# Performance work log

Measured on AMD Instinct MI355X. Metric: run time of the kernel, lower is better.

## Reference

```python
import jax, jax.numpy as jnp
import numpy as np

TAU = 1.0            # temperature (self.temperature.item())
FAST_WEIGHT_DECAY = 0.01
FAST_WEIGHT_LR = 0.01

B, IN, H = 128, 1024, 1024


def setup_inputs() -> dict:
    key = jax.random.key(0)
    k = jax.random.split(key, 6)
    scale_ih = 1.0 / np.sqrt(IN)
    scale_hh = np.sqrt(2.0 / (H + H))  # xavier_uniform-like std
    return {
        "x_t": jax.random.normal(k[0], (B, IN), jnp.float32),
        "h_prev": jax.random.normal(k[1], (B, H), jnp.float32),
        "W_ih": jax.random.normal(k[2], (H, IN), jnp.float32) * scale_ih,
        "b_ih": jnp.zeros((H,), jnp.float32),
        "W_hh_fixed": jax.random.normal(k[3], (H, H), jnp.float32) * scale_hh,
        "W_hh_virtual": jnp.zeros((H, H), jnp.float32),
        "gumbel_u": jax.random.uniform(k[4], (B, H, H), jnp.float32),
    }


def reference(x_t, h_prev, W_ih, b_ih, W_hh_fixed, W_hh_virtual, gumbel_u):
    # input contribution: Linear(input_size, hidden_size)
    input_contrib = x_t @ W_ih.T + b_ih                      # (B, H)

    # logits scaled by temperature once, then gumbel_softmax divides by tau again
    logits = (W_hh_fixed + W_hh_virtual) / TAU               # (H, H)
    eps = 1e-9
    g = -jnp.log(-jnp.log(jnp.clip(gumbel_u, eps, 1.0 - eps)))  # Gumbel(0,1), (B,H,H)
    y = jax.nn.softmax((logits[None, :, :] + g) / TAU, axis=2)  # soft sampling, (B,H,H)

    # weighted exchange: each output neuron o reduces sampled weights against h_prev
    contrib = jnp.einsum('boh,bh->bo', y, h_prev)            # (B, H)
    h_next = jnp.tanh(input_contrib + contrib)               # (B, H)

    # Hebbian fast-weight update (no_grad in original)
    hebbian = jnp.einsum('bo,bh->oh', h_next, h_prev) / B    # mean over batch, (H,H)
    W_hh_virtual_new = jax.lax.stop_gradient(
        W_hh_virtual * (1.0 - FAST_WEIGHT_DECAY) + hebbian * FAST_WEIGHT_LR
    )
    return h_next, W_hh_virtual_new
```

## Files before the change

kernel.cpp:

```cpp
#include <hip/hip_runtime.h>
#include <hip/hip_bf16.h>
#include <cstddef>

#define B_DIM  128
#define IN_DIM 1024
#define H_DIM  1024

constexpr float kDecay   = 1.0f - 0.01f;
constexpr float kLrOverB = 0.01f / 128.0f;

__global__ __launch_bounds__(256) void exp_logits(
    const float* __restrict__ W_f,
    const float* __restrict__ W_v,
    float* __restrict__ E)
{
    const int i = blockIdx.x * 256 + threadIdx.x;
    const float4 a = reinterpret_cast<const float4*>(W_f)[i];
    const float4 b = reinterpret_cast<const float4*>(W_v)[i];
    float4 e;
    e.x = __expf(a.x + b.x); e.y = __expf(a.y + b.y);
    e.z = __expf(a.z + b.z); e.w = __expf(a.w + b.w);
    reinterpret_cast<float4*>(E)[i] = e;
}

__global__ __launch_bounds__(256) void input_gemm(
    const float* __restrict__ x_t,
    const float* __restrict__ W_ih,
    const float* __restrict__ b_ih,
    float* __restrict__ ic)
{
    const int o0 = blockIdx.x * 64;
    const int b0 = blockIdx.y * 16;
    const int t  = threadIdx.x;

    __shared__ float Wt[64][68];
    __shared__ float xs[64][17];

    const int tx = t & 15;
    const int ty = t >> 4;

    float acc[4] = {0.f, 0.f, 0.f, 0.f};

    for (int kc = 0; kc < IN_DIM / 64; ++kc) {
        const int k0 = kc * 64;

#pragma unroll
        for (int ii = 0; ii < 4; ++ii) {
            const int i  = t + 256 * ii;
            const int r  = i >> 4;
            const int c4 = (i & 15) * 4;
            const float4 wv = *reinterpret_cast<const float4*>(
                &W_ih[(size_t)(o0 + r) * IN_DIM + k0 + c4]);
            Wt[c4 + 0][r] = wv.x; Wt[c4 + 1][r] = wv.y;
            Wt[c4 + 2][r] = wv.z; Wt[c4 + 3][r] = wv.w;
        }
        {
            const int br = t >> 4;
            const int c4 = (t & 15) * 4;
            const float4 xv = *reinterpret_cast<const float4*>(
                &x_t[(size_t)(b0 + br) * IN_DIM + k0 + c4]);
            xs[c4 + 0][br] = xv.x; xs[c4 + 1][br] = xv.y;
            xs[c4 + 2][br] = xv.z; xs[c4 + 3][br] = xv.w;
        }
        __syncthreads();

#pragma unroll 8
        for (int k = 0; k < 64; ++k) {
            const float  xb = xs[k][ty];
            const float4 wv = *reinterpret_cast<const float4*>(&Wt[k][4 * tx]);
            acc[0] = fmaf(wv.x, xb, acc[0]);
            acc[1] = fmaf(wv.y, xb, acc[1]);
            acc[2] = fmaf(wv.z, xb, acc[2]);
            acc[3] = fmaf(wv.w, xb, acc[3]);
        }
        __syncthreads();
    }

    const int o = o0 + 4 * tx;
    const int b = b0 + ty;
    float4 r;
    r.x = acc[0] + b_ih[o + 0];
    r.y = acc[1] + b_ih[o + 1];
    r.z = acc[2] + b_ih[o + 2];
    r.w = acc[3] + b_ih[o + 3];
    *reinterpret_cast<float4*>(&ic[(size_t)b * H_DIM + o]) = r;
}

__global__ __launch_bounds__(256) void fused_rows(
    const float* __restrict__ h_prev,
    const float* __restrict__ E,
    const float* __restrict__ gu,
    const float* __restrict__ ic,
    float* __restrict__ h_next)
{
    const int b    = blockIdx.y;
    const int t    = threadIdx.x;
    const int w    = t >> 6;
    const int lane = t & 63;
    const int ob   = blockIdx.x * 32 + w * 8;

    const float4* hp4 = reinterpret_cast<const float4*>(h_prev + (size_t)b * H_DIM);
    float4 hp[4];
#pragma unroll
    for (int j = 0; j < 4; ++j) hp[j] = hp4[lane + 64 * j];

    const float4* g4 = reinterpret_cast<const float4*>(gu + ((size_t)b * H_DIM + ob) * H_DIM);
    const float4* e4 = reinterpret_cast<const float4*>(E + (size_t)ob * H_DIM);

    float s[8], d[8];

#pragma unroll
    for (int r = 0; r < 8; ++r) {
        float sum = 0.f, dot = 0.f;
#pragma unroll
        for (int j = 0; j < 4; ++j) {
            const int idx = r * 256 + lane + 64 * j;
            const float4 u = g4[idx];
            const float4 e = e4[idx];
            const float4 p = hp[j];

            const float q0 = __fdividef(e.x, -__log2f(fmaxf(u.x, 1e-9f)));
            const float q1 = __fdividef(e.y, -__log2f(fmaxf(u.y, 1e-9f)));
            const float q2 = __fdividef(e.z, -__log2f(fmaxf(u.z, 1e-9f)));
            const float q3 = __fdividef(e.w, -__log2f(fmaxf(u.w, 1e-9f)));

            sum += (q0 + q1) + (q2 + q3);
            dot = fmaf(q0, p.x, dot);
            dot = fmaf(q1, p.y, dot);
            dot = fmaf(q2, p.z, dot);
            dot = fmaf(q3, p.w, dot);
        }
        s[r] = sum;
        d[r] = dot;
    }

#pragma unroll
    for (int off = 32; off > 0; off >>= 1) {
#pragma unroll
        for (int r = 0; r < 8; ++r) {
            s[r] += __shfl_xor(s[r], off, 64);
            d[r] += __shfl_xor(d[r], off, 64);
        }
    }

    if (lane == 0) {
        const size_t base = (size_t)b * H_DIM + ob;
        const float4 i0 = *reinterpret_cast<const float4*>(ic + base);
        const float4 i1 = *reinterpret_cast<const float4*>(ic + base + 4);
        float4 r0, r1;
        r0.x = tanhf(i0.x + __fdividef(d[0], s[0]));
        r0.y = tanhf(i0.y + __fdividef(d[1], s[1]));
        r0.z = tanhf(i0.z + __fdividef(d[2], s[2]));
        r0.w = tanhf(i0.w + __fdividef(d[3], s[3]));
        r1.x = tanhf(i1.x + __fdividef(d[4], s[4]));
        r1.y = tanhf(i1.y + __fdividef(d[5], s[5]));
        r1.z = tanhf(i1.z + __fdividef(d[6], s[6]));
        r1.w = tanhf(i1.w + __fdividef(d[7], s[7]));
        *reinterpret_cast<float4*>(h_next + base)     = r0;
        *reinterpret_cast<float4*>(h_next + base + 4) = r1;
    }
}

__global__ __launch_bounds__(256) void hebbian_update(
    const float* __restrict__ h_next,
    const float* __restrict__ h_prev,
    const float* __restrict__ W_v,
    float* __restrict__ W_out)
{
    const int h0 = blockIdx.x * 64;
    const int o0 = blockIdx.y * 64;
    const int t  = threadIdx.x;

    __shared__ __align__(16) float hn_s[B_DIM][64];
    __shared__ __align__(16) float hp_s[B_DIM][64];

#pragma unroll
    for (int i = 0; i < 32; ++i) {
        const int e  = t + 256 * i;
        const int bb = e >> 6;
        const int cc = e & 63;
        hn_s[bb][cc] = h_next[(size_t)bb * H_DIM + o0 + cc];
        hp_s[bb][cc] = h_prev[(size_t)bb * H_DIM + h0 + cc];
    }
    __syncthreads();

    const int tx = t & 15;
    const int ty = t >> 4;

    float acc[4][4] = {{0.f}};

#pragma unroll 8
    for (int b = 0; b < B_DIM; ++b) {
        const float4 av = reinterpret_cast<const float4*>(hn_s[b])[ty];
        const float4 bv = reinterpret_cast<const float4*>(hp_s[b])[tx];
        const float aa[4] = {av.x, av.y, av.z, av.w};
        const float bb[4] = {bv.x, bv.y, bv.z, bv.w};
#pragma unroll
        for (int a = 0; a < 4; ++a)
#pragma unroll
            for (int c = 0; c < 4; ++c)
                acc[a][c] = fmaf(aa[a], bb[c], acc[a][c]);
    }

#pragma unroll
    for (int a = 0; a < 4; ++a) {
        const int o = o0 + 4 * ty + a;
        const size_t base = (size_t)o * H_DIM + h0 + 4 * tx;
        const float4 wv = *reinterpret_cast<const float4*>(W_v + base);
        float4 r;
        r.x = wv.x * kDecay + acc[a][0] * kLrOverB;
        r.y = wv.y * kDecay + acc[a][1] * kLrOverB;
        r.z = wv.z * kDecay + acc[a][2] * kLrOverB;
        r.w = wv.w * kDecay + acc[a][3] * kLrOverB;
        *reinterpret_cast<float4*>(W_out + base) = r;
    }
}

extern "C" void kernel_launch(void* const* d_in, const int* in_sizes, int n_in,
                              void* d_out, int out_size, void* d_ws, size_t ws_size,
                              hipStream_t stream)
{
    const float* x_t    = (const float*)d_in[0];
    const float* h_prev = (const float*)d_in[1];
    const float* W_ih   = (const float*)d_in[2];
    const float* b_ih   = (const float*)d_in[3];
    const float* W_f    = (const float*)d_in[4];
    const float* W_v    = (const float*)d_in[5];
    const float* gu     = (const float*)d_in[6];

    float* out    = (float*)d_out;
    float* h_next = out;
    float* W_out  = out + (size_t)B_DIM * H_DIM;

    float* E  = (float*)d_ws;
    float* ic = E + (size_t)H_DIM * H_DIM;

    exp_logits<<<dim3(H_DIM * H_DIM / 1024), 256, 0, stream>>>(W_f, W_v, E);

    input_gemm<<<dim3(H_DIM / 64, B_DIM / 16), 256, 0, stream>>>(
        x_t, W_ih, b_ih, ic);

    fused_rows<<<dim3(H_DIM / 32, B_DIM), 256, 0, stream>>>(
        h_prev, E, gu, ic, h_next);

    hebbian_update<<<dim3(H_DIM / 64, H_DIM / 64), 256, 0, stream>>>(
        h_next, h_prev, W_v, W_out);
}
```

Baseline: 162.1 us.

## Reuse E rows across batches in fused_rows and stream gumbel with nontemporal loads

```diff
diff --git a/kernel.cpp b/kernel.cpp
--- a/kernel.cpp
+++ b/kernel.cpp
@@ -8,6 +8,8 @@
 
 constexpr float kDecay   = 1.0f - 0.01f;
 constexpr float kLrOverB = 0.01f / 128.0f;
+
+typedef float f32x4 __attribute__((ext_vector_type(4)));
 
 __global__ __launch_bounds__(256) void exp_logits(
     const float* __restrict__ W_f,
@@ -93,71 +95,90 @@
     const float* __restrict__ ic,
     float* __restrict__ h_next)
 {
-    const int b    = blockIdx.y;
-    const int t    = threadIdx.x;
-    const int w    = t >> 6;
-    const int lane = t & 63;
-    const int ob   = blockIdx.x * 32 + w * 8;
-
-    const float4* hp4 = reinterpret_cast<const float4*>(h_prev + (size_t)b * H_DIM);
-    float4 hp[4];
-#pragma unroll
-    for (int j = 0; j < 4; ++j) hp[j] = hp4[lane + 64 * j];
-
-    const float4* g4 = reinterpret_cast<const float4*>(gu + ((size_t)b * H_DIM + ob) * H_DIM);
-    const float4* e4 = reinterpret_cast<const float4*>(E + (size_t)ob * H_DIM);
-
-    float s[8], d[8];
-
-#pragma unroll
-    for (int r = 0; r < 8; ++r) {
-        float sum = 0.f, dot = 0.f;
-#pragma unroll
-        for (int j = 0; j < 4; ++j) {
-            const int idx = r * 256 + lane + 64 * j;
-            const float4 u = g4[idx];
-            const float4 e = e4[idx];
-            const float4 p = hp[j];
-
-            const float q0 = __fdividef(e.x, -__log2f(fmaxf(u.x, 1e-9f)));
-            const float q1 = __fdividef(e.y, -__log2f(fmaxf(u.y, 1e-9f)));
-            const float q2 = __fdividef(e.z, -__log2f(fmaxf(u.z, 1e-9f)));
-            const float q3 = __fdividef(e.w, -__log2f(fmaxf(u.w, 1e-9f)));
-
-            sum += (q0 + q1) + (q2 + q3);
-            dot = fmaf(q0, p.x, dot);
-            dot = fmaf(q1, p.y, dot);
-            dot = fmaf(q2, p.z, dot);
-            dot = fmaf(q3, p.w, dot);
-        }
-        s[r] = sum;
-        d[r] = dot;
-    }
-
-#pragma unroll
-    for (int off = 32; off > 0; off >>= 1) {
-#pragma unroll
-        for (int r = 0; r < 8; ++r) {
-            s[r] += __shfl_xor(s[r], off, 64);
-            d[r] += __shfl_xor(d[r], off, 64);
-        }
-    }
-
-    if (lane == 0) {
-        const size_t base = (size_t)b * H_DIM + ob;
-        const float4 i0 = *reinterpret_cast<const float4*>(ic + base);
-        const float4 i1 = *reinterpret_cast<const float4*>(ic + base + 4);
-        float4 r0, r1;
-        r0.x = tanhf(i0.x + __fdividef(d[0], s[0]));
-        r0.y = tanhf(i0.y + __fdividef(d[1], s[1]));
-        r0.z = tanhf(i0.z + __fdividef(d[2], s[2]));
-        r0.w = tanhf(i0.w + __fdividef(d[3], s[3]));
-        r1.x = tanhf(i1.x + __fdividef(d[4], s[4]));
-        r1.y = tanhf(i1.y + __fdividef(d[5], s[5]));
-        r1.z = tanhf(i1.z + __fdividef(d[6], s[6]));
-        r1.w = tanhf(i1.w + __fdividef(d[7], s[7]));
-        *reinterpret_cast<float4*>(h_next + base)     = r0;
-        *reinterpret_cast<float4*>(h_next + base + 4) = r1;
+    const int b0 = blockIdx.x * 8;
+    const int o0 = blockIdx.y * 16;
+    const int t  = threadIdx.x;
+    const int w  = t >> 6, lane = t & 63;
+
+    __shared__ __align__(16) float hp_s[8 * H_DIM];
+
+    {
+        const float4* src = reinterpret_cast<const float4*>(h_prev) + (size_t)b0 * 256;
+        float4*       dst = reinterpret_cast<float4*>(hp_s);
+#pragma unroll
+        for (int ii = 0; ii < 8; ++ii) dst[t + 256 * ii] = src[t + 256 * ii];
+    }
+    __syncthreads();
+
+    const int orow0 = o0 + w * 4;
+
+    float4 e[4][4];
+    {
+        const float4* E4 = reinterpret_cast<const float4*>(E) + (size_t)orow0 * 256;
+#pragma unroll
+        for (int r = 0; r < 4; ++r)
+#pragma unroll
+            for (int j = 0; j < 4; ++j)
+                e[r][j] = E4[r * 256 + lane + 64 * j];
+    }
+
+    const float4* hp4 = reinterpret_cast<const float4*>(hp_s);
+
+    for (int bb = 0; bb < 8; ++bb) {
+        const int b = b0 + bb;
+        const f32x4* g4 = reinterpret_cast<const f32x4*>(gu)
+                        + ((size_t)b * H_DIM + orow0) * 256;
+
+        f32x4 u[4][4];
+#pragma unroll
+        for (int r = 0; r < 4; ++r)
+#pragma unroll
+            for (int j = 0; j < 4; ++j)
+                u[r][j] = __builtin_nontemporal_load(g4 + (r * 4 + j) * 64 + lane);
+
+        float4 p[4];
+#pragma unroll
+        for (int j = 0; j < 4; ++j) p[j] = hp4[bb * 256 + lane + 64 * j];
+
+        float s[4], d[4];
+#pragma unroll
+        for (int r = 0; r < 4; ++r) {
+            float sum = 0.f, dot = 0.f;
+#pragma unroll
+            for (int j = 0; j < 4; ++j) {
+                const f32x4 uu = u[r][j];
+                const float4 ee = e[r][j];
+                const float4 pp = p[j];
+                const float q0 = __fdividef(ee.x, -__log2f(fmaxf(uu.x, 1e-9f)));
+                const float q1 = __fdividef(ee.y, -__log2f(fmaxf(uu.y, 1e-9f)));
+                const float q2 = __fdividef(ee.z, -__log2f(fmaxf(uu.z, 1e-9f)));
+                const float q3 = __fdividef(ee.w, -__log2f(fmaxf(uu.w, 1e-9f)));
+                sum += (q0 + q1) + (q2 + q3);
+                dot = fmaf(q0, pp.x, dot);
+                dot = fmaf(q1, pp.y, dot);
+                dot = fmaf(q2, pp.z, dot);
+                dot = fmaf(q3, pp.w, dot);
+            }
+            s[r] = sum;
+            d[r] = dot;
+        }
+
+#pragma unroll
+        for (int off = 32; off > 0; off >>= 1) {
+#pragma unroll
+            for (int r = 0; r < 4; ++r) {
+                s[r] += __shfl_xor(s[r], off, 64);
+                d[r] += __shfl_xor(d[r], off, 64);
+            }
+        }
+
+        if (lane == 0) {
+#pragma unroll
+            for (int r = 0; r < 4; ++r) {
+                const size_t idx = (size_t)b * H_DIM + orow0 + r;
+                h_next[idx] = tanhf(ic[idx] + __fdividef(d[r], s[r]));
+            }
+        }
     }
 }
 
@@ -240,7 +261,7 @@
     input_gemm<<<dim3(H_DIM / 64, B_DIM / 16), 256, 0, stream>>>(
         x_t, W_ih, b_ih, ic);
 
-    fused_rows<<<dim3(H_DIM / 32, B_DIM), 256, 0, stream>>>(
+    fused_rows<<<dim3(B_DIM / 8, H_DIM / 16), 256, 0, stream>>>(
         h_prev, E, gu, ic, h_next);
 
     hebbian_update<<<dim3(H_DIM / 64, H_DIM / 64), 256, 0, stream>>>(
```

New measurement: 154.9 us. -4.5%, faster.
